# Kernel optimization log

Hardware: AMD Instinct MI355X
Metric: run time of the kernel (lower is better)

The kernel has to match this reference:

```python
import jax, jax.numpy as jnp
import numpy as np

KS = 7           # kernel spatial size (odd)
OMEGA0 = 10.0    # SIREN frequency
PAD = 3          # conv padding ('same' for ks=7)


def _rel_positions_grid(ks):
    # [2, ks, ks], coords in [-1, 1]
    lin = jnp.linspace(-1.0, 1.0, ks, dtype=jnp.float32)
    yy, xx = jnp.meshgrid(lin, lin, indexing='ij')
    return jnp.stack([yy, xx], axis=0)


def _siren(points, W1, b1, W2, b2, W3, b3):
    # points: [..., 3] -> [..., out_ch*in_ch]
    h = jnp.sin(OMEGA0 * (points @ W1 + b1))
    h = jnp.sin(OMEGA0 * (h @ W2 + b2))
    return h @ W3 + b3


def setup_inputs() -> dict:
    key = jax.random.key(0)
    ks = jax.random.split(key, 8)
    B, Cin, Cout, G, H, W, Hid = 16, 32, 32, 8, 64, 64, 32
    x = jax.random.normal(ks[0], (B, Cin, G, H, W), dtype=jnp.float32)
    # deterministic rotation grid on SO(2): angles in [0, 2pi)
    input_g_elems = (jnp.arange(G, dtype=jnp.float32) * (2.0 * jnp.pi / G))[None, :]
    # SIREN params: 3 -> Hid -> Hid -> Cout*Cin
    W1 = jax.random.uniform(ks[1], (3, Hid), minval=-1.0, maxval=1.0) / 3.0
    b1 = jnp.zeros((Hid,), jnp.float32)
    c = jnp.sqrt(6.0 / Hid) / OMEGA0
    W2 = jax.random.uniform(ks[2], (Hid, Hid), minval=-c, maxval=c)
    b2 = jnp.zeros((Hid,), jnp.float32)
    W3 = jax.random.uniform(ks[3], (Hid, Cout * Cin), minval=-c, maxval=c)
    b3 = jnp.zeros((Cout * Cin,), jnp.float32)
    bias = jnp.zeros((1, Cout), jnp.float32)
    return {"x": x, "input_g_elems": input_g_elems, "W1": W1, "b1": b1,
            "W2": W2, "b2": b2, "W3": W3, "b3": b3, "bias": bias}


def reference(x, input_g_elems, W1, b1, W2, b2, W3, b3, bias):
    B, Cin, Gin, H, Wd = x.shape
    Cout = bias.shape[1]
    two_pi = 2.0 * jnp.pi
    rel_pos = _rel_positions_grid(KS)                        # [2, ks, ks]

    # deterministic / non-partial path: g_elems = input_g_elems
    thetas = input_g_elems[0]                                # [G]
    Gout = thetas.shape[0]

    # acted group coords: inv(g) . h = (h - g) mod 2pi, normalized to [-1, 1)
    acted_g = jnp.mod(thetas[None, :] - thetas[:, None], two_pi) / jnp.pi - 1.0  # [Gout, Gin]

    # rotate Rd rel positions by inv(g) = R(-theta)
    ct, st = jnp.cos(-thetas), jnp.sin(-thetas)
    R = jnp.stack([jnp.stack([ct, -st], -1), jnp.stack([st, ct], -1)], -2)  # [Gout,2,2]
    acted_rel = jnp.einsum('gij,jhw->gihw', R, rel_pos)      # [Gout,2,ks,ks]

    # positions fed to kernel net: [Gout, Gin, ks, ks, 3]
    pos_rd = jnp.broadcast_to(acted_rel[:, :, None], (Gout, 2, Gin, KS, KS))
    pos_g = jnp.broadcast_to(acted_g[:, None, :, None, None], (Gout, 1, Gin, KS, KS))
    coords = jnp.concatenate([pos_rd, pos_g], axis=1)        # [Gout,3,Gin,ks,ks]
    points = jnp.moveaxis(coords, 1, -1)                     # [Gout,Gin,ks,ks,3]

    kernel = _siren(points, W1, b1, W2, b2, W3, b3)          # [Gout,Gin,ks,ks,Cout*Cin]
    kernel = kernel.reshape(Gout, Gin, KS, KS, Cout, Cin)
    kernel = jnp.transpose(kernel, (0, 4, 5, 1, 2, 3))       # [Gout,Cout,Cin,Gin,ks,ks]

    # zero kernel outside unit disk of (rotated) Rd positions
    mask = (jnp.linalg.norm(acted_rel, axis=1) <= 1.0)       # [Gout,ks,ks]
    kernel = kernel * mask[:, None, None, None, :, :]

    weight = kernel.reshape(Gout * Cout, Cin * Gin, KS, KS)
    x2 = x.reshape(B, Cin * Gin, H, Wd)
    out = jax.lax.conv_general_dilated(
        x2, weight, window_strides=(1, 1), padding=[(PAD, PAD), (PAD, PAD)],
        dimension_numbers=('NCHW', 'OIHW', 'NCHW'))          # [B, Gout*Cout, H, W]
    out = out.reshape(B, Gout, Cout, H, Wd).transpose(0, 2, 1, 3, 4)  # [B,Cout,Gout,H,W]
    out = out + bias.reshape(1, Cout, 1, 1, 1)
    return out
```

## Files before the change

kernel.cpp:

```cpp
#include <hip/hip_runtime.h>
#include <math.h>

typedef __bf16 bf16_t;
typedef __bf16 bf16x8 __attribute__((ext_vector_type(8)));
typedef float  f32x4  __attribute__((ext_vector_type(4)));

#define B_    16
#define CIN_  32
#define COUT_ 32
#define G_    8
#define CH_   256
#define H_    64
#define W_    64
#define HID_  32
#define KS_   7
#define PAD_  3
#define WP_   70

#define ROW_ELEMS  (WP_ * CH_)
#define XP_ELEMS   ((size_t)B_ * WP_ * ROW_ELEMS)
#define XP_BYTES   (XP_ELEMS * 2)

#define GENW_BLOCKS   (G_ * KS_ * KS_)
#define REPACK_BLOCKS (B_ * (H_ + 6))
#define CONV_BLOCKS   (B_ * (H_ / 2))

static __device__ __forceinline__ unsigned pack_bf16(float a, float b) {
    union { __bf16 h; unsigned short u; } ua, ub;
    ua.h = (__bf16)a; ub.h = (__bf16)b;
    return (unsigned)ua.u | ((unsigned)ub.u << 16);
}

static __device__ __forceinline__ void dma16(const bf16_t* g, bf16_t* l) {
    __builtin_amdgcn_global_load_lds(
        (const __attribute__((address_space(1))) void*)g,
        (__attribute__((address_space(3))) void*)l, 16, 0, 0);
}

__global__ void prep(const float* __restrict__ x, bf16_t* __restrict__ xp,
                     const float* __restrict__ thetas,
                     const float* __restrict__ W1, const float* __restrict__ b1,
                     const float* __restrict__ W2, const float* __restrict__ b2,
                     const float* __restrict__ W3, const float* __restrict__ b3,
                     bf16_t* __restrict__ w2out) {
    __shared__ float h1s[8][33];
    __shared__ float h2s[8][33];
    int tid = threadIdx.x;
    if (blockIdx.x < GENW_BLOCKS) {
        int blk = blockIdx.x;
        int gout = blk / 49, p = blk - gout * 49;
        int ky = p / 7, kx = p - ky * 7;
        const float TWO_PI = 6.283185307179586f;
        const float PI_F   = 3.14159265358979323846f;
        float th_o = thetas[gout];
        float ct = cosf(-th_o), st = sinf(-th_o);
        float yy = (float)(ky - 3) / 3.0f;
        float xx = (float)(kx - 3) / 3.0f;
        float r0 = ct * yy - st * xx;
        float r1 = st * yy + ct * xx;
        float maskv = (r0 * r0 + r1 * r1 <= 1.00001f) ? 1.0f : 0.0f;

        int gin = tid >> 5, j = tid & 31;
        {
            float th_i = thetas[gin];
            float d = fmodf(th_i - th_o, TWO_PI);
            if (d < 0.0f) d += TWO_PI;
            float ag = d / PI_F - 1.0f;
            float a = r0 * W1[j] + r1 * W1[32 + j] + ag * W1[64 + j] + b1[j];
            h1s[gin][j] = __sinf(10.0f * a);
        }
        __syncthreads();
        {
            float a = b2[j];
            #pragma unroll
            for (int i = 0; i < HID_; ++i) a += h1s[gin][i] * W2[i * HID_ + j];
            h2s[gin][j] = __sinf(10.0f * a);
        }
        __syncthreads();
        for (int rep = 0; rep < 4; ++rep) {
            int o = rep * 256 + tid;
            float w3c[HID_];
            #pragma unroll
            for (int i = 0; i < HID_; ++i) w3c[i] = W3[i * 1024 + o];
            float bb = b3[o];
            int cout = o >> 5, cin = o & 31;
            union { bf16x8 v; bf16_t e[8]; } o8;
            #pragma unroll
            for (int g = 0; g < 8; ++g) {
                float a = bb;
                #pragma unroll
                for (int i = 0; i < HID_; ++i) a += h2s[g][i] * w3c[i];
                o8.e[g] = (bf16_t)(a * maskv);
            }
            size_t base = ((size_t)p * 8192 + (size_t)cin * 256
                           + (size_t)(gout * COUT_ + cout)) * 8;
            *reinterpret_cast<bf16x8*>(w2out + base) = o8.v;
        }
        return;
    }
    int blk = blockIdx.x - GENW_BLOCKS;
    int b = blk / (H_ + 6), hy = blk % (H_ + 6);
    const int4 z4 = make_int4(0, 0, 0, 0);
    if (hy >= H_) {
        int idx = hy - H_;
        int y = (idx < 3) ? idx : idx + 64;
        bf16_t* dst = xp + ((size_t)(b * WP_) + y) * ROW_ELEMS;
        for (int i = tid; i < ROW_ELEMS / 8; i += 256)
            *reinterpret_cast<int4*>(dst + (size_t)i * 8) = z4;
        return;
    }
    int lane = tid & 63, wv = tid >> 6;
    int r = lane >> 3;
    int t = lane & 7;
    size_t orow = ((size_t)(b * WP_) + (hy + 3)) * ROW_ELEMS;
    for (int it = 0; it < 8; ++it) {
        int c0 = wv * 8 + it * 32;
        const float* src = x + ((size_t)(b * CH_ + c0 + r)) * (H_ * W_)
                             + (size_t)hy * W_ + t * 8;
        float4 f0 = *reinterpret_cast<const float4*>(src);
        float4 f1 = *reinterpret_cast<const float4*>(src + 4);
        int d0 = (int)pack_bf16(f0.x, f0.y);
        int d1 = (int)pack_bf16(f0.z, f0.w);
        int d2 = (int)pack_bf16(f1.x, f1.y);
        int d3 = (int)pack_bf16(f1.z, f1.w);
        int p0, p1, p2, p3;
        p0 = __shfl_xor(d0, 32); p1 = __shfl_xor(d1, 32);
        p2 = __shfl_xor(d2, 32); p3 = __shfl_xor(d3, 32);
        if ((r & 4) == 0) { d2 = p0; d3 = p1; } else { d0 = p2; d1 = p3; }
        p0 = __shfl_xor(d0, 16); p1 = __shfl_xor(d1, 16);
        p2 = __shfl_xor(d2, 16); p3 = __shfl_xor(d3, 16);
        if ((r & 2) == 0) { d1 = p0; d3 = p2; } else { d0 = p1; d2 = p3; }
        p0 = __shfl_xor(d0, 8); p1 = __shfl_xor(d1, 8);
        p2 = __shfl_xor(d2, 8); p3 = __shfl_xor(d3, 8);
        if ((r & 1) == 0) {
            d0 = (d0 & 0xFFFF) | (p0 << 16);
            d1 = (d1 & 0xFFFF) | (p1 << 16);
            d2 = (d2 & 0xFFFF) | (p2 << 16);
            d3 = (d3 & 0xFFFF) | (p3 << 16);
        } else {
            d0 = (d0 & 0xFFFF0000) | ((unsigned)p0 >> 16);
            d1 = (d1 & 0xFFFF0000) | ((unsigned)p1 >> 16);
            d2 = (d2 & 0xFFFF0000) | ((unsigned)p2 >> 16);
            d3 = (d3 & 0xFFFF0000) | ((unsigned)p3 >> 16);
        }
        int xpos = t * 8 + r + 3;
        int c16 = c0 >> 3;
        int4 v = make_int4(d0, d1, d2, d3);
        *reinterpret_cast<int4*>(xp + orow + ((size_t)c16 * WP_ + xpos) * 8) = v;
    }
    if (tid < 192) {
        int col = tid >> 5, cg = tid & 31;
        int xx = (col < 3) ? col : col + 64;
        *reinterpret_cast<int4*>(xp + orow + ((size_t)cg * WP_ + xx) * 8) = z4;
    }
}

#define CONV_STEP(USE, PRE, SS)                                               \
  do {                                                                        \
    int sl = (SS) + 1, kyn = ky;                                              \
    if (sl == 56) { sl = 0; kyn = ky + 1; if (kyn == 7) { kyn = 6; sl = 55; } }\
    int tapn = kyn * 7 + (sl >> 3), kcn = sl & 7;                             \
    const bf16_t* wpn = w2 + ((size_t)(tapn * 32 + lq) * 256 + nbase) * 8     \
                        + (size_t)kcn * (4 * 256 * 8);                        \
    PRE[0] = *reinterpret_cast<const bf16x8*>(wpn);                           \
    PRE[1] = *reinterpret_cast<const bf16x8*>(wpn + 128);                     \
    PRE[2] = *reinterpret_cast<const bf16x8*>(wpn + 256);                     \
    PRE[3] = *reinterpret_cast<const bf16x8*>(wpn + 384);                     \
    int kx = (SS) >> 3, kc = (SS) & 7;                                        \
    int cb = (kc * 4 + lq) * WP_;                                             \
    bf16x8 afrag[8];                                                          \
    _Pragma("unroll")                                                         \
    for (int mt = 0; mt < 4; ++mt) {                                          \
      int xr = mt * 16 + lm + kx;                                             \
      afrag[mt]     = *reinterpret_cast<const bf16x8*>(&slotA[(cb + xr) * 8]);\
      afrag[mt + 4] = *reinterpret_cast<const bf16x8*>(&slotB[(cb + xr) * 8]);\
    }                                                                         \
    _Pragma("unroll")                                                         \
    for (int mt = 0; mt < 8; ++mt)                                            \
      _Pragma("unroll")                                                       \
      for (int nt = 0; nt < 4; ++nt)                                          \
        acc[mt][nt] = __builtin_amdgcn_mfma_f32_16x16x32_bf16(                \
            afrag[mt], USE[nt], acc[mt][nt], 0, 0, 0);                        \
  } while (0)

__launch_bounds__(256, 2)
__global__ void conv_mfma(const bf16_t* __restrict__ xp,
                          const bf16_t* __restrict__ w2,
                          const float* __restrict__ bias,
                          float* __restrict__ out) {
    __shared__ __align__(16) bf16_t lds[2][ROW_ELEMS];
    int blk = blockIdx.x;
    int b = blk >> 5, h0 = (blk & 31) << 1;
    int tid = threadIdx.x;
    int ns = tid >> 6, lane = tid & 63;
    int lm = lane & 15, lq = lane >> 4;
    int nbase = ns * 64 + lm;

    f32x4 acc[8][4];
    #pragma unroll
    for (int i = 0; i < 8; ++i)
        #pragma unroll
        for (int j = 0; j < 4; ++j) {
            f32x4 z = {0.0f, 0.0f, 0.0f, 0.0f};
            acc[i][j] = z;
        }

    const bf16_t* rows = xp + (((size_t)(b * WP_) + h0)) * ROW_ELEMS;
    for (int c = ns; c < 70; c += 4)
        dma16(rows + (size_t)c * 512 + lane * 8, &lds[0][0] + c * 512);

    bf16x8 bcur[4], bnxt[4];
    {
        const bf16_t* wp0 = w2 + ((size_t)lq * 256 + nbase) * 8;
        bcur[0] = *reinterpret_cast<const bf16x8*>(wp0);
        bcur[1] = *reinterpret_cast<const bf16x8*>(wp0 + 128);
        bcur[2] = *reinterpret_cast<const bf16x8*>(wp0 + 256);
        bcur[3] = *reinterpret_cast<const bf16x8*>(wp0 + 384);
    }
    __syncthreads();

    for (int ky = 0; ky < KS_; ++ky) {
        const bf16_t* slotA = &lds[ky & 1][0];
        const bf16_t* slotB = &lds[(ky + 1) & 1][0];
        #pragma unroll 1
        for (int s = 0; s < 56; s += 2) {
            CONV_STEP(bcur, bnxt, s);
            CONV_STEP(bnxt, bcur, s + 1);
        }
        if (ky < KS_ - 1) {
            __syncthreads();
            bf16_t* dstslot = &lds[ky & 1][0];
            const bf16_t* src = rows + (size_t)(ky + 2) * ROW_ELEMS;
            for (int c = ns; c < 35; c += 4)
                dma16(src + (size_t)c * 512 + lane * 8, dstslot + c * 512);
            __syncthreads();
        }
    }

    #pragma unroll
    for (int mt = 0; mt < 8; ++mt) {
        int h = h0 + (mt >> 2);
        int wq = (mt & 3) * 16 + lq * 4;
        #pragma unroll
        for (int nt = 0; nt < 4; ++nt) {
            int n = ns * 64 + nt * 16 + lm;
            int gout = n >> 5, cout = n & 31;
            float bv = bias[cout];
            f32x4 v = acc[mt][nt];
            v[0] += bv; v[1] += bv; v[2] += bv; v[3] += bv;
            float* po = out + (((size_t)(b * COUT_ + cout) * G_ + gout) * (H_ * W_)
                               + h * W_ + wq);
            *reinterpret_cast<f32x4*>(po) = v;
        }
    }
}

extern "C" void kernel_launch(void* const* d_in, const int* in_sizes, int n_in,
                              void* d_out, int out_size, void* d_ws, size_t ws_size,
                              hipStream_t stream) {
    const float* x      = (const float*)d_in[0];
    const float* thetas = (const float*)d_in[1];
    const float* W1     = (const float*)d_in[2];
    const float* b1     = (const float*)d_in[3];
    const float* W2     = (const float*)d_in[4];
    const float* b2     = (const float*)d_in[5];
    const float* W3     = (const float*)d_in[6];
    const float* b3     = (const float*)d_in[7];
    const float* bias   = (const float*)d_in[8];
    float* out = (float*)d_out;

    bf16_t* xp = (bf16_t*)d_ws;
    bf16_t* w2 = (bf16_t*)((char*)d_ws + XP_BYTES);

    hipLaunchKernelGGL(prep, dim3(GENW_BLOCKS + REPACK_BLOCKS), dim3(256), 0, stream,
                       x, xp, thetas, W1, b1, W2, b2, W3, b3, w2);
    hipLaunchKernelGGL(conv_mfma, dim3(CONV_BLOCKS), dim3(256), 0, stream,
                       xp, w2, bias, out);
}
```

Measured before the change: 544.9 us.

## Software-pipeline LDS A-fragment loads and restructure weight layout per tap

The conv inner loop now prefetches both the A fragments from LDS and the B weight fragments one step ahead, double-buffering them in registers instead of loading A synchronously before each MFMA batch. The weight layout written by the generator is rearranged to a per-tap contiguous block with channel-chunk stride, which makes the per-step address arithmetic constant offsets. s_setprio is raised around the MFMA block to favour the matrix issue. The cost is higher register pressure from the extra A buffers, which risks spills or lower occupancy under the launch bound of 2.

```diff
diff --git a/kernel.cpp b/kernel.cpp
--- a/kernel.cpp
+++ b/kernel.cpp
@@ -77,13 +77,15 @@
             h2s[gin][j] = __sinf(10.0f * a);
         }
         __syncthreads();
+        #pragma unroll 1
         for (int rep = 0; rep < 4; ++rep) {
             int o = rep * 256 + tid;
+            int cout = o & 31, cin = o >> 5;
+            int col = cout * 32 + cin;
             float w3c[HID_];
             #pragma unroll
-            for (int i = 0; i < HID_; ++i) w3c[i] = W3[i * 1024 + o];
-            float bb = b3[o];
-            int cout = o >> 5, cin = o & 31;
+            for (int i = 0; i < HID_; ++i) w3c[i] = W3[i * 1024 + col];
+            float bb = b3[col];
             union { bf16x8 v; bf16_t e[8]; } o8;
             #pragma unroll
             for (int g = 0; g < 8; ++g) {
@@ -92,8 +94,8 @@
                 for (int i = 0; i < HID_; ++i) a += h2s[g][i] * w3c[i];
                 o8.e[g] = (bf16_t)(a * maskv);
             }
-            size_t base = ((size_t)p * 8192 + (size_t)cin * 256
-                           + (size_t)(gout * COUT_ + cout)) * 8;
+            size_t base = (size_t)p * 65536 + (size_t)cin * 2048
+                        + (size_t)(gout * COUT_ + cout) * 8;
             *reinterpret_cast<bf16x8*>(w2out + base) = o8.v;
         }
         return;
@@ -155,32 +157,27 @@
     }
 }
 
-#define CONV_STEP(USE, PRE, SS)                                               \
+#define CONV_STEP(AC, AN, BC, BN, PC, PB, AOF)                                \
   do {                                                                        \
-    int sl = (SS) + 1, kyn = ky;                                              \
-    if (sl == 56) { sl = 0; kyn = ky + 1; if (kyn == 7) { kyn = 6; sl = 55; } }\
-    int tapn = kyn * 7 + (sl >> 3), kcn = sl & 7;                             \
-    const bf16_t* wpn = w2 + ((size_t)(tapn * 32 + lq) * 256 + nbase) * 8     \
-                        + (size_t)kcn * (4 * 256 * 8);                        \
-    PRE[0] = *reinterpret_cast<const bf16x8*>(wpn);                           \
-    PRE[1] = *reinterpret_cast<const bf16x8*>(wpn + 128);                     \
-    PRE[2] = *reinterpret_cast<const bf16x8*>(wpn + 256);                     \
-    PRE[3] = *reinterpret_cast<const bf16x8*>(wpn + 384);                     \
-    int kx = (SS) >> 3, kc = (SS) & 7;                                        \
-    int cb = (kc * 4 + lq) * WP_;                                             \
-    bf16x8 afrag[8];                                                          \
+    _Pragma("unroll")                                                         \
+    for (int nt = 0; nt < 4; ++nt)                                            \
+      BN[nt] = *reinterpret_cast<const bf16x8*>(                              \
+          (PB) + wlane_off + (PC) * 8192 + nt * 128);                         \
     _Pragma("unroll")                                                         \
     for (int mt = 0; mt < 4; ++mt) {                                          \
-      int xr = mt * 16 + lm + kx;                                             \
-      afrag[mt]     = *reinterpret_cast<const bf16x8*>(&slotA[(cb + xr) * 8]);\
-      afrag[mt + 4] = *reinterpret_cast<const bf16x8*>(&slotB[(cb + xr) * 8]);\
+      AN[mt]     = *reinterpret_cast<const bf16x8*>(                          \
+          aA + ((PC) * 4 * WP_ + mt * 16) * 8 + (AOF));                       \
+      AN[mt + 4] = *reinterpret_cast<const bf16x8*>(                          \
+          aB + ((PC) * 4 * WP_ + mt * 16) * 8 + (AOF));                       \
     }                                                                         \
+    __builtin_amdgcn_s_setprio(1);                                            \
     _Pragma("unroll")                                                         \
     for (int mt = 0; mt < 8; ++mt)                                            \
       _Pragma("unroll")                                                       \
       for (int nt = 0; nt < 4; ++nt)                                          \
         acc[mt][nt] = __builtin_amdgcn_mfma_f32_16x16x32_bf16(                \
-            afrag[mt], USE[nt], acc[mt][nt], 0, 0, 0);                        \
+            AC[mt], BC[nt], acc[mt][nt], 0, 0, 0);                            \
+    __builtin_amdgcn_s_setprio(0);                                            \
   } while (0)
 
 __launch_bounds__(256, 2)
@@ -194,7 +191,7 @@
     int tid = threadIdx.x;
     int ns = tid >> 6, lane = tid & 63;
     int lm = lane & 15, lq = lane >> 4;
-    int nbase = ns * 64 + lm;
+    int wlane_off = lq * 2048 + (ns * 64 + lm) * 8;
 
     f32x4 acc[8][4];
     #pragma unroll
@@ -210,22 +207,35 @@
         dma16(rows + (size_t)c * 512 + lane * 8, &lds[0][0] + c * 512);
 
     bf16x8 bcur[4], bnxt[4];
-    {
-        const bf16_t* wp0 = w2 + ((size_t)lq * 256 + nbase) * 8;
-        bcur[0] = *reinterpret_cast<const bf16x8*>(wp0);
-        bcur[1] = *reinterpret_cast<const bf16x8*>(wp0 + 128);
-        bcur[2] = *reinterpret_cast<const bf16x8*>(wp0 + 256);
-        bcur[3] = *reinterpret_cast<const bf16x8*>(wp0 + 384);
-    }
+    #pragma unroll
+    for (int nt = 0; nt < 4; ++nt)
+        bcur[nt] = *reinterpret_cast<const bf16x8*>(w2 + wlane_off + nt * 128);
     __syncthreads();
 
     for (int ky = 0; ky < KS_; ++ky) {
         const bf16_t* slotA = &lds[ky & 1][0];
         const bf16_t* slotB = &lds[(ky + 1) & 1][0];
+        bf16x8 acur[8], anxt[8];
+        #pragma unroll
+        for (int mt = 0; mt < 4; ++mt) {
+            int xr = (lq * WP_ + lm) * 8 + mt * 128;
+            acur[mt]     = *reinterpret_cast<const bf16x8*>(&slotA[xr]);
+            acur[mt + 4] = *reinterpret_cast<const bf16x8*>(&slotB[xr]);
+        }
         #pragma unroll 1
-        for (int s = 0; s < 56; s += 2) {
-            CONV_STEP(bcur, bnxt, s);
-            CONV_STEP(bnxt, bcur, s + 1);
+        for (int kx = 0; kx < 7; ++kx) {
+            const bf16_t* wkx = w2 + (size_t)(ky * 7 + kx) * 65536;
+            const bf16_t* wnx = (ky == 6 && kx == 6) ? wkx : wkx + 65536;
+            const bf16_t* aA = slotA + (lq * WP_ + lm + kx) * 8;
+            const bf16_t* aB = slotB + (lq * WP_ + lm + kx) * 8;
+            CONV_STEP(acur, anxt, bcur, bnxt, 1, wkx, 0);
+            CONV_STEP(anxt, acur, bnxt, bcur, 2, wkx, 0);
+            CONV_STEP(acur, anxt, bcur, bnxt, 3, wkx, 0);
+            CONV_STEP(anxt, acur, bnxt, bcur, 4, wkx, 0);
+            CONV_STEP(acur, anxt, bcur, bnxt, 5, wkx, 0);
+            CONV_STEP(anxt, acur, bnxt, bcur, 6, wkx, 0);
+            CONV_STEP(acur, anxt, bcur, bnxt, 7, wkx, 0);
+            CONV_STEP(anxt, acur, bnxt, bcur, 0, wnx, 8);
         }
         if (ky < KS_ - 1) {
             __syncthreads();
```

After: 534.5 us. Within noise of the previous version (-1.9%).
